# Kernel tuning notes

Measured on AMD Instinct MI355X. Metric: run time of the kernel, lower is better.

Reference implementation:

```python
import jax, jax.numpy as jnp
import numpy as np

TOP_K = 2


def setup_inputs() -> dict:
    key = jax.random.key(0)
    ks = jax.random.split(key, 7)
    B, S, D, E = 8, 2048, 1024, 8
    scale = 1.0 / np.sqrt(D)
    return {
        "X": jax.random.normal(ks[0], (B, S, D), dtype=jnp.float32),
        "We": jax.random.normal(ks[1], (E, D, D), dtype=jnp.float32) * scale,
        "be": jax.random.normal(ks[2], (E, D), dtype=jnp.float32) * scale,
        "Wr": jax.random.normal(ks[3], (E, D), dtype=jnp.float32) * scale,
        "br": jax.random.normal(ks[4], (E,), dtype=jnp.float32) * scale,
        "Wo": jax.random.normal(ks[5], (D, D), dtype=jnp.float32) * scale,
        "bo": jax.random.normal(ks[6], (D,), dtype=jnp.float32) * scale,
    }


def reference(X, We, be, Wr, br, Wo, bo):
    # Router: logits [B, S, E] -> softmax -> top-k
    router_logits = jnp.einsum("bsd,ed->bse", X, Wr) + br
    router_weights = jax.nn.softmax(router_logits, axis=-1)
    top_k_weights, top_k_indices = jax.lax.top_k(router_weights, TOP_K)  # [B,S,K]

    # Every expert Linear applied to all tokens (matches original's dense-per-expert math).
    # expert_outputs: [B, S, E, D]
    expert_outputs = jnp.einsum("bsd,ehd->bseh", X, We) + be

    # Gather the top-k experts per token and combine with router weights.
    # gathered: [B, S, K, D]
    gathered = jnp.take_along_axis(expert_outputs, top_k_indices[..., None], axis=2)
    combined = jnp.sum(top_k_weights[..., None] * gathered, axis=2)  # [B, S, D]

    # Output projection
    out = jnp.einsum("bsd,hd->bsh", combined, Wo) + bo
    return out
```

## Files before the change

### kernel.cpp

```cpp
#include <hip/hip_runtime.h>
#include <stdint.h>

#define T_TOK 16384
#define D_DIM 1024
#define E_NUM 8
#define NTILE 136

typedef __attribute__((ext_vector_type(4))) float f32x4;
typedef __attribute__((ext_vector_type(8))) __bf16 bf16x8;
typedef __attribute__((ext_vector_type(4))) unsigned short u16x4;
typedef const __attribute__((address_space(1))) void* gas_ptr;
typedef __attribute__((address_space(3))) void* las_ptr;

#define WS_Y     0ULL
#define WS_ATOK  67108864ULL
#define WS_AW    (WS_ATOK + 131072ULL)
#define WS_SCHED (WS_AW + 131072ULL)
#define WS_TMP   (WS_SCHED + 8192ULL)
#define WS_TKI   WS_TMP
#define WS_TKW   (WS_TKI + 131072ULL)
#define WS_CNTS  (WS_TKW + 131072ULL)
#define WS_BASE  (WS_CNTS + 8192ULL)
#define WS_WOB   WS_TMP


__device__ __forceinline__ unsigned short f2b(float f){
  unsigned int u = __float_as_uint(f);
  u = (u + 0x7FFFu + ((u >> 16) & 1u)) >> 16;
  return (unsigned short)u;
}

__global__ __launch_bounds__(256) void k_router(const float* __restrict__ X,
    const float* __restrict__ Wr, const float* __restrict__ br,
    unsigned short* __restrict__ Xb, int* __restrict__ tki, float* __restrict__ tkw)
{
  const int wv = threadIdx.x >> 6, lane = threadIdx.x & 63;
  const int t = blockIdx.x * 4 + wv;
  const float* x = X + (size_t)t * D_DIM;
  unsigned short* xb = Xb + (size_t)t * D_DIM;
  float acc[E_NUM] = {};
  #pragma unroll
  for (int c = 0; c < 4; ++c){
    const int d = c * 256 + lane * 4;
    f32x4 xv = *reinterpret_cast<const f32x4*>(x + d);
    u16x4 o;
    o[0]=f2b(xv[0]); o[1]=f2b(xv[1]); o[2]=f2b(xv[2]); o[3]=f2b(xv[3]);
    *reinterpret_cast<u16x4*>(xb + d) = o;
    #pragma unroll
    for (int e = 0; e < E_NUM; ++e){
      f32x4 w4 = *reinterpret_cast<const f32x4*>(Wr + e * D_DIM + d);
      acc[e] += xv[0]*w4[0] + xv[1]*w4[1] + xv[2]*w4[2] + xv[3]*w4[3];
    }
  }
  #pragma unroll
  for (int e = 0; e < E_NUM; ++e){
    float v = acc[e];
    #pragma unroll
    for (int off = 32; off >= 1; off >>= 1) v += __shfl_xor(v, off, 64);
    acc[e] = v + br[e];
  }
  int i1 = 0; float l1 = acc[0];
  #pragma unroll
  for (int e = 1; e < E_NUM; ++e) if (acc[e] > l1){ l1 = acc[e]; i1 = e; }
  int i2 = -1; float l2 = -3.4e38f;
  #pragma unroll
  for (int e = 0; e < E_NUM; ++e) if (e != i1 && acc[e] > l2){ l2 = acc[e]; i2 = e; }
  float s = 0.f;
  #pragma unroll
  for (int e = 0; e < E_NUM; ++e) s += __expf(acc[e] - l1);
  if (lane == 0){
    tki[2*t] = i1; tki[2*t+1] = i2;
    tkw[2*t] = 1.0f / s; tkw[2*t+1] = __expf(l2 - l1) / s;
  }
}

__global__ void k_cvt(const float* __restrict__ in, unsigned short* __restrict__ out, int n4)
{
  int i = blockIdx.x * blockDim.x + threadIdx.x;
  if (i >= n4) return;
  f32x4 v = reinterpret_cast<const f32x4*>(in)[i];
  u16x4 o;
  o[0]=f2b(v[0]); o[1]=f2b(v[1]); o[2]=f2b(v[2]); o[3]=f2b(v[3]);
  reinterpret_cast<u16x4*>(out)[i] = o;
}

__global__ __launch_bounds__(64) void k_hist(const int* __restrict__ tki, int* __restrict__ cnts)
{
  const int b = blockIdx.x, lane = threadIdx.x;
  const int t = b * 64 + lane;
  const int e0 = tki[2*t], e1 = tki[2*t+1];
  #pragma unroll
  for (int ex = 0; ex < E_NUM; ++ex){
    unsigned long long m0 = __ballot(e0 == ex);
    unsigned long long m1 = __ballot(e1 == ex);
    if (lane == 0) cnts[b * E_NUM + ex] = __popcll(m0) + __popcll(m1);
  }
}

__global__ __launch_bounds__(64) void k_scan(const int* __restrict__ cnts,
    int* __restrict__ bases, int4* __restrict__ sched)
{
  const int lane = threadIdx.x;
  const int e = lane & 7, g = lane >> 3;
  int own = 0;
  for (int i = 0; i < 32; ++i) own += cnts[(g * 32 + i) * E_NUM + e];
  int incl = own;
  #pragma unroll
  for (int s = 8; s < 64; s <<= 1){
    int v = __shfl_up(incl, s, 64);
    if (lane >= s) incl += v;
  }
  int tot[E_NUM];
  #pragma unroll
  for (int ee = 0; ee < E_NUM; ++ee) tot[ee] = __shfl(incl, 56 + ee, 64);
  int offs_e = 0;
  #pragma unroll
  for (int ee = 0; ee < E_NUM; ++ee) if (ee < e) offs_e += tot[ee];
  int run = offs_e + (incl - own);
  for (int i = 0; i < 32; ++i){
    const int b = g * 32 + i;
    bases[b * E_NUM + e] = run;
    run += cnts[b * E_NUM + e];
  }
  if (lane == 0){
    int slot = 0, off = 0;
    for (int ee = 0; ee < E_NUM; ++ee){
      const int c = tot[ee];
      for (int tile = 0; tile * 256 < c && slot < NTILE; ++tile)
        sched[slot++] = make_int4(ee, off + tile * 256, min(256, c - tile * 256), 0);
      off += c;
    }
    while (slot < NTILE) sched[slot++] = make_int4(0, 0, 0, 0);
  }
}

__global__ __launch_bounds__(64) void k_scatter(const int* __restrict__ tki,
    const float* __restrict__ tkw, const int* __restrict__ bases,
    int* __restrict__ atok, float* __restrict__ aw)
{
  const int b = blockIdx.x, lane = threadIdx.x;
  const int t = b * 64 + lane;
  const unsigned long long lt = (1ull << lane) - 1ull;
  const int e0 = tki[2*t], e1 = tki[2*t+1];
  int r0 = 0, r1 = 0, p0c[E_NUM];
  #pragma unroll
  for (int ex = 0; ex < E_NUM; ++ex){
    unsigned long long m0 = __ballot(e0 == ex);
    p0c[ex] = __popcll(m0);
    if (e0 == ex) r0 = __popcll(m0 & lt);
  }
  #pragma unroll
  for (int ex = 0; ex < E_NUM; ++ex){
    unsigned long long m1 = __ballot(e1 == ex);
    if (e1 == ex) r1 = p0c[ex] + __popcll(m1 & lt);
  }
  const int row0 = bases[b * E_NUM + e0] + r0;
  const int row1 = bases[b * E_NUM + e1] + r1;
  atok[row0] = 2*t;     aw[row0] = tkw[2*t];
  atok[row1] = 2*t + 1; aw[row1] = tkw[2*t+1];
}

__global__ __launch_bounds__(512, 4) void k_expert(const unsigned short* __restrict__ Xb,
    const unsigned short* __restrict__ Web, const float* __restrict__ be,
    const int4* __restrict__ sched, const int* __restrict__ atok,
    const float* __restrict__ aw, unsigned short* __restrict__ Y)
{
  __shared__ unsigned short As[256 * 64];
  __shared__ unsigned short Bs[128 * 64];
  __shared__ int   tok_s[256];
  __shared__ float w_s[256];

  const int lin = blockIdx.x;
  const int x = lin & 7, c = (lin >> 3) & 7, a = lin >> 6;
  const int j = x * 17 + a;
  const int4 sc = sched[j];
  const int e = sc.x, row0 = sc.y, nval = sc.z;
  const int n0 = c * 128;

  const int tid = threadIdx.x, wv = tid >> 6, lane = tid & 63;
  const int wm = wv >> 1, wn = wv & 1, lr = lane & 15, lg = lane >> 4;

  if (tid < 256){
    tok_s[tid] = atok[row0 + max(0, min(tid, nval - 1))];
    w_s[tid]   = aw[row0 + min(tid, 255)];
  }
  __syncthreads();

  const char* asrc[4]; const char* bsrc[2]; int ldsoA[4], ldsoB[2];
  #pragma unroll
  for (int i = 0; i < 4; ++i){
    const int chunk = i * 8 + wv;
    const int byte0 = chunk * 1024 + lane * 16;
    const int r = byte0 >> 7;
    const int scb = (byte0 & 127) ^ ((r & 7) << 4);
    asrc[i] = (const char*)(Xb + (size_t)(tok_s[r] >> 1) * D_DIM) + scb;
    ldsoA[i] = chunk * 512;
  }
  #pragma unroll
  for (int i = 0; i < 2; ++i){
    const int chunk = i * 8 + wv;
    const int byte0 = chunk * 1024 + lane * 16;
    const int r = byte0 >> 7;
    const int scb = (byte0 & 127) ^ ((r & 7) << 4);
    bsrc[i] = (const char*)(Web + ((size_t)e * D_DIM + n0 + r) * D_DIM) + scb;
    ldsoB[i] = chunk * 512;
  }

  f32x4 acc[4][4] = {};
  #pragma unroll 1
  for (int kt = 0; kt < 16; ++kt){
    __syncthreads();
    #pragma unroll
    for (int i = 0; i < 4; ++i)
      __builtin_amdgcn_global_load_lds((gas_ptr)(asrc[i] + kt * 128), (las_ptr)(As + ldsoA[i]), 16, 0, 0);
    #pragma unroll
    for (int i = 0; i < 2; ++i)
      __builtin_amdgcn_global_load_lds((gas_ptr)(bsrc[i] + kt * 128), (las_ptr)(Bs + ldsoB[i]), 16, 0, 0);
    __syncthreads();
    #pragma unroll
    for (int kk = 0; kk < 2; ++kk){
      bf16x8 af[4], bfr[4];
      #pragma unroll
      for (int fm = 0; fm < 4; ++fm){
        const int r = wm*64 + fm*16 + lr;
        af[fm] = *reinterpret_cast<const bf16x8*>((char*)As + ((r*128 + kk*64 + lg*16) ^ ((r & 7) << 4)));
      }
      #pragma unroll
      for (int fn = 0; fn < 4; ++fn){
        const int r = wn*64 + fn*16 + lr;
        bfr[fn] = *reinterpret_cast<const bf16x8*>((char*)Bs + ((r*128 + kk*64 + lg*16) ^ ((r & 7) << 4)));
      }
      #pragma unroll
      for (int fm = 0; fm < 4; ++fm)
        #pragma unroll
        for (int fn = 0; fn < 4; ++fn)
          acc[fm][fn] = __builtin_amdgcn_mfma_f32_16x16x32_bf16(af[fm], bfr[fn], acc[fm][fn], 0, 0, 0);
    }
  }

  float bev[4];
  #pragma unroll
  for (int fn = 0; fn < 4; ++fn) bev[fn] = be[e * D_DIM + n0 + wn*64 + fn*16 + lr];
  #pragma unroll
  for (int fm = 0; fm < 4; ++fm){
    #pragma unroll
    for (int jj = 0; jj < 4; ++jj){
      const int r = wm*64 + fm*16 + lg*4 + jj;
      if (r < nval){
        const float w = w_s[r];
        const size_t yrow = (size_t)tok_s[r];
        #pragma unroll
        for (int fn = 0; fn < 4; ++fn){
          const int col = n0 + wn*64 + fn*16 + lr;
          Y[yrow * D_DIM + col] = f2b(w * (acc[fm][fn][jj] + bev[fn]));
        }
      }
    }
  }
}

__global__ __launch_bounds__(512, 4) void k_outproj(const unsigned short* __restrict__ Y,
    const unsigned short* __restrict__ Wob, const float* __restrict__ bo,
    float* __restrict__ out)
{
  __shared__ unsigned short As0[256 * 64];
  __shared__ unsigned short As1[256 * 64];
  __shared__ unsigned short Bs[128 * 64];

  const int lin = blockIdx.x;
  const int x = lin & 7, c = (lin >> 3) & 7, a = lin >> 6;
  const int tm = x * 8 + a;
  const int n0 = c * 128;

  const int tid = threadIdx.x, wv = tid >> 6, lane = tid & 63;
  const int wm = wv >> 1, wn = wv & 1, lr = lane & 15, lg = lane >> 4;

  const char* a0src[4]; const char* a1src[4]; const char* bsrc[2]; int ldsoA[4], ldsoB[2];
  #pragma unroll
  for (int i = 0; i < 4; ++i){
    const int chunk = i * 8 + wv;
    const int byte0 = chunk * 1024 + lane * 16;
    const int r = byte0 >> 7;
    const int scb = (byte0 & 127) ^ ((r & 7) << 4);
    const size_t t = (size_t)(tm * 256 + r);
    a0src[i] = (const char*)(Y + (2*t)     * D_DIM) + scb;
    a1src[i] = (const char*)(Y + (2*t + 1) * D_DIM) + scb;
    ldsoA[i] = chunk * 512;
  }
  #pragma unroll
  for (int i = 0; i < 2; ++i){
    const int chunk = i * 8 + wv;
    const int byte0 = chunk * 1024 + lane * 16;
    const int r = byte0 >> 7;
    const int scb = (byte0 & 127) ^ ((r & 7) << 4);
    bsrc[i] = (const char*)(Wob + (size_t)(n0 + r) * D_DIM) + scb;
    ldsoB[i] = chunk * 512;
  }

  f32x4 acc[4][4] = {};
  #pragma unroll 1
  for (int kt = 0; kt < 16; ++kt){
    __syncthreads();
    #pragma unroll
    for (int i = 0; i < 4; ++i){
      __builtin_amdgcn_global_load_lds((gas_ptr)(a0src[i] + kt * 128), (las_ptr)(As0 + ldsoA[i]), 16, 0, 0);
      __builtin_amdgcn_global_load_lds((gas_ptr)(a1src[i] + kt * 128), (las_ptr)(As1 + ldsoA[i]), 16, 0, 0);
    }
    #pragma unroll
    for (int i = 0; i < 2; ++i)
      __builtin_amdgcn_global_load_lds((gas_ptr)(bsrc[i] + kt * 128), (las_ptr)(Bs + ldsoB[i]), 16, 0, 0);
    __syncthreads();
    #pragma unroll
    for (int kk = 0; kk < 2; ++kk){
      bf16x8 a0f[4], a1f[4], bfr[4];
      #pragma unroll
      for (int fm = 0; fm < 4; ++fm){
        const int r = wm*64 + fm*16 + lr;
        const int ba = (r*128 + kk*64 + lg*16) ^ ((r & 7) << 4);
        a0f[fm] = *reinterpret_cast<const bf16x8*>((char*)As0 + ba);
        a1f[fm] = *reinterpret_cast<const bf16x8*>((char*)As1 + ba);
      }
      #pragma unroll
      for (int fn = 0; fn < 4; ++fn){
        const int r = wn*64 + fn*16 + lr;
        bfr[fn] = *reinterpret_cast<const bf16x8*>((char*)Bs + ((r*128 + kk*64 + lg*16) ^ ((r & 7) << 4)));
      }
      #pragma unroll
      for (int fm = 0; fm < 4; ++fm)
        #pragma unroll
        for (int fn = 0; fn < 4; ++fn){
          acc[fm][fn] = __builtin_amdgcn_mfma_f32_16x16x32_bf16(a0f[fm], bfr[fn], acc[fm][fn], 0, 0, 0);
          acc[fm][fn] = __builtin_amdgcn_mfma_f32_16x16x32_bf16(a1f[fm], bfr[fn], acc[fm][fn], 0, 0, 0);
        }
    }
  }

  float bov[4];
  #pragma unroll
  for (int fn = 0; fn < 4; ++fn) bov[fn] = bo[n0 + wn*64 + fn*16 + lr];
  #pragma unroll
  for (int fm = 0; fm < 4; ++fm){
    #pragma unroll
    for (int jj = 0; jj < 4; ++jj){
      const int r = wm*64 + fm*16 + lg*4 + jj;
      #pragma unroll
      for (int fn = 0; fn < 4; ++fn){
        const int col = n0 + wn*64 + fn*16 + lr;
        out[(size_t)(tm * 256 + r) * D_DIM + col] = acc[fm][fn][jj] + bov[fn];
      }
    }
  }
}

extern "C" void kernel_launch(void* const* d_in, const int* in_sizes, int n_in,
                              void* d_out, int out_size, void* d_ws, size_t ws_size,
                              hipStream_t stream)
{
  const float* X  = (const float*)d_in[0];
  const float* We = (const float*)d_in[1];
  const float* be = (const float*)d_in[2];
  const float* Wr = (const float*)d_in[3];
  const float* br = (const float*)d_in[4];
  const float* Wo = (const float*)d_in[5];
  const float* bo = (const float*)d_in[6];
  float* out = (float*)d_out;
  char* ws = (char*)d_ws;

  unsigned short* Y   = (unsigned short*)(ws + WS_Y);
  int*   atok  = (int*)(ws + WS_ATOK);
  float* aw    = (float*)(ws + WS_AW);
  int4*  sched = (int4*)(ws + WS_SCHED);
  int*   tki   = (int*)(ws + WS_TKI);
  float* tkw   = (float*)(ws + WS_TKW);
  int*   cnts  = (int*)(ws + WS_CNTS);
  int*   bases = (int*)(ws + WS_BASE);
  unsigned short* Wob = (unsigned short*)(ws + WS_WOB);

  unsigned short* Xb  = (unsigned short*)d_out;
  unsigned short* Web = (unsigned short*)((char*)d_out + 33554432);

  k_router<<<T_TOK / 4, 256, 0, stream>>>(X, Wr, br, Xb, tki, tkw);
  k_cvt<<<(E_NUM * D_DIM * D_DIM / 4) / 256, 256, 0, stream>>>(We, Web, E_NUM * D_DIM * D_DIM / 4);
  k_hist<<<256, 64, 0, stream>>>(tki, cnts);
  k_scan<<<1, 64, 0, stream>>>(cnts, bases, sched);
  k_scatter<<<256, 64, 0, stream>>>(tki, tkw, bases, atok, aw);
  k_cvt<<<(D_DIM * D_DIM / 4) / 256, 256, 0, stream>>>(Wo, Wob, D_DIM * D_DIM / 4);
  k_expert<<<NTILE * 8, 512, 0, stream>>>(Xb, Web, be, sched, atok, aw, Y);
  k_outproj<<<512, 512, 0, stream>>>(Y, Wob, bo, out);
}
```

Before: 333.8 us.

## Fuse router and weight conversions; merge routing schedule kernels into one block

Combines the router, expert-weight and output-weight bf16 conversions into a single launch, and folds histogram, scan and scatter into one single-block kernel using shared memory. Expert tiles with no tokens now exit early. Router weights are staged as bf16 to shrink workspace. This reduces launch count and inter-kernel gaps, at the cost of a serial single-block scheduling step and slightly lower precision of combine weights.

```diff
diff --git a/kernel.cpp b/kernel.cpp
--- a/kernel.cpp
+++ b/kernel.cpp
@@ -16,12 +16,9 @@
 #define WS_ATOK  67108864ULL
 #define WS_AW    (WS_ATOK + 131072ULL)
 #define WS_SCHED (WS_AW + 131072ULL)
-#define WS_TMP   (WS_SCHED + 8192ULL)
-#define WS_TKI   WS_TMP
-#define WS_TKW   (WS_TKI + 131072ULL)
-#define WS_CNTS  (WS_TKW + 131072ULL)
-#define WS_BASE  (WS_CNTS + 8192ULL)
-#define WS_WOB   WS_TMP
+#define WS_TKI   (WS_SCHED + 2304ULL)
+#define WS_TKWH  (WS_TKI + 131072ULL)
+#define WS_WOB   (WS_TKWH + 65536ULL)
 
 
 __device__ __forceinline__ unsigned short f2b(float f){
@@ -29,135 +26,153 @@
   u = (u + 0x7FFFu + ((u >> 16) & 1u)) >> 16;
   return (unsigned short)u;
 }
-
-__global__ __launch_bounds__(256) void k_router(const float* __restrict__ X,
+__device__ __forceinline__ float b2f(unsigned short u){
+  return __uint_as_float(((unsigned int)u) << 16);
+}
+
+__global__ __launch_bounds__(256) void k_prep(const float* __restrict__ X,
     const float* __restrict__ Wr, const float* __restrict__ br,
-    unsigned short* __restrict__ Xb, int* __restrict__ tki, float* __restrict__ tkw)
+    const float* __restrict__ We, const float* __restrict__ Wo,
+    unsigned short* __restrict__ Xb, unsigned short* __restrict__ Web,
+    unsigned short* __restrict__ Wob, int* __restrict__ tki, unsigned short* __restrict__ tkwh)
 {
-  const int wv = threadIdx.x >> 6, lane = threadIdx.x & 63;
-  const int t = blockIdx.x * 4 + wv;
-  const float* x = X + (size_t)t * D_DIM;
-  unsigned short* xb = Xb + (size_t)t * D_DIM;
-  float acc[E_NUM] = {};
-  #pragma unroll
-  for (int c = 0; c < 4; ++c){
-    const int d = c * 256 + lane * 4;
-    f32x4 xv = *reinterpret_cast<const f32x4*>(x + d);
+  const int bid = blockIdx.x;
+  if (bid < 4096){
+    const int wv = threadIdx.x >> 6, lane = threadIdx.x & 63;
+    const int t = bid * 4 + wv;
+    const float* x = X + (size_t)t * D_DIM;
+    unsigned short* xb = Xb + (size_t)t * D_DIM;
+    float acc[E_NUM] = {};
+    #pragma unroll
+    for (int c = 0; c < 4; ++c){
+      const int d = c * 256 + lane * 4;
+      f32x4 xv = *reinterpret_cast<const f32x4*>(x + d);
+      u16x4 o;
+      o[0]=f2b(xv[0]); o[1]=f2b(xv[1]); o[2]=f2b(xv[2]); o[3]=f2b(xv[3]);
+      *reinterpret_cast<u16x4*>(xb + d) = o;
+      #pragma unroll
+      for (int e = 0; e < E_NUM; ++e){
+        f32x4 w4 = *reinterpret_cast<const f32x4*>(Wr + e * D_DIM + d);
+        acc[e] += xv[0]*w4[0] + xv[1]*w4[1] + xv[2]*w4[2] + xv[3]*w4[3];
+      }
+    }
+    #pragma unroll
+    for (int e = 0; e < E_NUM; ++e){
+      float v = acc[e];
+      #pragma unroll
+      for (int off = 32; off >= 1; off >>= 1) v += __shfl_xor(v, off, 64);
+      acc[e] = v + br[e];
+    }
+    int i1 = 0; float l1 = acc[0];
+    #pragma unroll
+    for (int e = 1; e < E_NUM; ++e) if (acc[e] > l1){ l1 = acc[e]; i1 = e; }
+    int i2 = -1; float l2 = -3.4e38f;
+    #pragma unroll
+    for (int e = 0; e < E_NUM; ++e) if (e != i1 && acc[e] > l2){ l2 = acc[e]; i2 = e; }
+    float s = 0.f;
+    #pragma unroll
+    for (int e = 0; e < E_NUM; ++e) s += __expf(acc[e] - l1);
+    if (lane == 0){
+      tki[2*t] = i1; tki[2*t+1] = i2;
+      tkwh[2*t] = f2b(1.0f / s); tkwh[2*t+1] = f2b(__expf(l2 - l1) / s);
+    }
+  } else if (bid < 12288){
+    const int i = (bid - 4096) * 256 + threadIdx.x;
+    f32x4 v = reinterpret_cast<const f32x4*>(We)[i];
     u16x4 o;
-    o[0]=f2b(xv[0]); o[1]=f2b(xv[1]); o[2]=f2b(xv[2]); o[3]=f2b(xv[3]);
-    *reinterpret_cast<u16x4*>(xb + d) = o;
-    #pragma unroll
-    for (int e = 0; e < E_NUM; ++e){
-      f32x4 w4 = *reinterpret_cast<const f32x4*>(Wr + e * D_DIM + d);
-      acc[e] += xv[0]*w4[0] + xv[1]*w4[1] + xv[2]*w4[2] + xv[3]*w4[3];
-    }
-  }
-  #pragma unroll
-  for (int e = 0; e < E_NUM; ++e){
-    float v = acc[e];
-    #pragma unroll
-    for (int off = 32; off >= 1; off >>= 1) v += __shfl_xor(v, off, 64);
-    acc[e] = v + br[e];
-  }
-  int i1 = 0; float l1 = acc[0];
-  #pragma unroll
-  for (int e = 1; e < E_NUM; ++e) if (acc[e] > l1){ l1 = acc[e]; i1 = e; }
-  int i2 = -1; float l2 = -3.4e38f;
-  #pragma unroll
-  for (int e = 0; e < E_NUM; ++e) if (e != i1 && acc[e] > l2){ l2 = acc[e]; i2 = e; }
-  float s = 0.f;
-  #pragma unroll
-  for (int e = 0; e < E_NUM; ++e) s += __expf(acc[e] - l1);
-  if (lane == 0){
-    tki[2*t] = i1; tki[2*t+1] = i2;
-    tkw[2*t] = 1.0f / s; tkw[2*t+1] = __expf(l2 - l1) / s;
-  }
-}
-
-__global__ void k_cvt(const float* __restrict__ in, unsigned short* __restrict__ out, int n4)
-{
-  int i = blockIdx.x * blockDim.x + threadIdx.x;
-  if (i >= n4) return;
-  f32x4 v = reinterpret_cast<const f32x4*>(in)[i];
-  u16x4 o;
-  o[0]=f2b(v[0]); o[1]=f2b(v[1]); o[2]=f2b(v[2]); o[3]=f2b(v[3]);
-  reinterpret_cast<u16x4*>(out)[i] = o;
-}
-
-__global__ __launch_bounds__(64) void k_hist(const int* __restrict__ tki, int* __restrict__ cnts)
-{
-  const int b = blockIdx.x, lane = threadIdx.x;
-  const int t = b * 64 + lane;
-  const int e0 = tki[2*t], e1 = tki[2*t+1];
-  #pragma unroll
-  for (int ex = 0; ex < E_NUM; ++ex){
-    unsigned long long m0 = __ballot(e0 == ex);
-    unsigned long long m1 = __ballot(e1 == ex);
-    if (lane == 0) cnts[b * E_NUM + ex] = __popcll(m0) + __popcll(m1);
-  }
-}
-
-__global__ __launch_bounds__(64) void k_scan(const int* __restrict__ cnts,
-    int* __restrict__ bases, int4* __restrict__ sched)
-{
-  const int lane = threadIdx.x;
-  const int e = lane & 7, g = lane >> 3;
-  int own = 0;
-  for (int i = 0; i < 32; ++i) own += cnts[(g * 32 + i) * E_NUM + e];
-  int incl = own;
-  #pragma unroll
-  for (int s = 8; s < 64; s <<= 1){
-    int v = __shfl_up(incl, s, 64);
-    if (lane >= s) incl += v;
-  }
-  int tot[E_NUM];
-  #pragma unroll
-  for (int ee = 0; ee < E_NUM; ++ee) tot[ee] = __shfl(incl, 56 + ee, 64);
-  int offs_e = 0;
-  #pragma unroll
-  for (int ee = 0; ee < E_NUM; ++ee) if (ee < e) offs_e += tot[ee];
-  int run = offs_e + (incl - own);
-  for (int i = 0; i < 32; ++i){
-    const int b = g * 32 + i;
-    bases[b * E_NUM + e] = run;
-    run += cnts[b * E_NUM + e];
-  }
-  if (lane == 0){
-    int slot = 0, off = 0;
-    for (int ee = 0; ee < E_NUM; ++ee){
-      const int c = tot[ee];
-      for (int tile = 0; tile * 256 < c && slot < NTILE; ++tile)
-        sched[slot++] = make_int4(ee, off + tile * 256, min(256, c - tile * 256), 0);
-      off += c;
-    }
-    while (slot < NTILE) sched[slot++] = make_int4(0, 0, 0, 0);
-  }
-}
-
-__global__ __launch_bounds__(64) void k_scatter(const int* __restrict__ tki,
-    const float* __restrict__ tkw, const int* __restrict__ bases,
+    o[0]=f2b(v[0]); o[1]=f2b(v[1]); o[2]=f2b(v[2]); o[3]=f2b(v[3]);
+    reinterpret_cast<u16x4*>(Web)[i] = o;
+  } else {
+    const int i = (bid - 12288) * 256 + threadIdx.x;
+    f32x4 v = reinterpret_cast<const f32x4*>(Wo)[i];
+    u16x4 o;
+    o[0]=f2b(v[0]); o[1]=f2b(v[1]); o[2]=f2b(v[2]); o[3]=f2b(v[3]);
+    reinterpret_cast<u16x4*>(Wob)[i] = o;
+  }
+}
+
+__global__ __launch_bounds__(1024) void k_sched2(const int* __restrict__ tki,
+    const unsigned short* __restrict__ tkwh, int4* __restrict__ sched,
     int* __restrict__ atok, float* __restrict__ aw)
 {
-  const int b = blockIdx.x, lane = threadIdx.x;
-  const int t = b * 64 + lane;
-  const unsigned long long lt = (1ull << lane) - 1ull;
-  const int e0 = tki[2*t], e1 = tki[2*t+1];
-  int r0 = 0, r1 = 0, p0c[E_NUM];
-  #pragma unroll
-  for (int ex = 0; ex < E_NUM; ++ex){
-    unsigned long long m0 = __ballot(e0 == ex);
-    p0c[ex] = __popcll(m0);
-    if (e0 == ex) r0 = __popcll(m0 & lt);
-  }
-  #pragma unroll
-  for (int ex = 0; ex < E_NUM; ++ex){
-    unsigned long long m1 = __ballot(e1 == ex);
-    if (e1 == ex) r1 = p0c[ex] + __popcll(m1 & lt);
-  }
-  const int row0 = bases[b * E_NUM + e0] + r0;
-  const int row1 = bases[b * E_NUM + e1] + r1;
-  atok[row0] = 2*t;     aw[row0] = tkw[2*t];
-  atok[row1] = 2*t + 1; aw[row1] = tkw[2*t+1];
+  __shared__ int cnts[256][E_NUM];
+  __shared__ int bases[256][E_NUM];
+  const int tid = threadIdx.x, wv = tid >> 6, lane = tid & 63;
+
+  #pragma unroll 1
+  for (int i = 0; i < 16; ++i){
+    const int g = wv * 16 + i;
+    const int t = g * 64 + lane;
+    const int e0 = tki[2*t], e1 = tki[2*t+1];
+    #pragma unroll
+    for (int ex = 0; ex < E_NUM; ++ex){
+      unsigned long long m0 = __ballot(e0 == ex);
+      unsigned long long m1 = __ballot(e1 == ex);
+      if (lane == 0) cnts[g][ex] = __popcll(m0) + __popcll(m1);
+    }
+  }
+  __syncthreads();
+
+  if (wv == 0){
+    const int e = lane & 7, g8 = lane >> 3;
+    int own = 0;
+    #pragma unroll 1
+    for (int i = 0; i < 32; ++i) own += cnts[g8 * 32 + i][e];
+    int incl = own;
+    #pragma unroll
+    for (int s = 8; s < 64; s <<= 1){
+      int v = __shfl_up(incl, s, 64);
+      if (lane >= s) incl += v;
+    }
+    int tot[E_NUM];
+    #pragma unroll
+    for (int ee = 0; ee < E_NUM; ++ee) tot[ee] = __shfl(incl, 56 + ee, 64);
+    int offs_e = 0;
+    #pragma unroll
+    for (int ee = 0; ee < E_NUM; ++ee) if (ee < e) offs_e += tot[ee];
+    int run = offs_e + (incl - own);
+    #pragma unroll 1
+    for (int i = 0; i < 32; ++i){
+      const int b = g8 * 32 + i;
+      bases[b][e] = run;
+      run += cnts[b][e];
+    }
+    if (lane == 0){
+      int slot = 0, off = 0;
+      for (int ee = 0; ee < E_NUM; ++ee){
+        const int c = tot[ee];
+        for (int tile = 0; tile * 256 < c && slot < NTILE; ++tile)
+          sched[slot++] = make_int4(ee, off + tile * 256, min(256, c - tile * 256), 0);
+        off += c;
+      }
+      while (slot < NTILE) sched[slot++] = make_int4(0, 0, 0, 0);
+    }
+  }
+  __syncthreads();
+
+  #pragma unroll 1
+  for (int i = 0; i < 16; ++i){
+    const int g = wv * 16 + i;
+    const int t = g * 64 + lane;
+    const unsigned long long lt = (1ull << lane) - 1ull;
+    const int e0 = tki[2*t], e1 = tki[2*t+1];
+    int r0 = 0, r1 = 0, p0c[E_NUM];
+    #pragma unroll
+    for (int ex = 0; ex < E_NUM; ++ex){
+      unsigned long long m0 = __ballot(e0 == ex);
+      p0c[ex] = __popcll(m0);
+      if (e0 == ex) r0 = __popcll(m0 & lt);
+    }
+    #pragma unroll
+    for (int ex = 0; ex < E_NUM; ++ex){
+      unsigned long long m1 = __ballot(e1 == ex);
+      if (e1 == ex) r1 = p0c[ex] + __popcll(m1 & lt);
+    }
+    const int row0 = bases[g][e0] + r0;
+    const int row1 = bases[g][e1] + r1;
+    atok[row0] = 2*t;     aw[row0] = b2f(tkwh[2*t]);
+    atok[row1] = 2*t + 1; aw[row1] = b2f(tkwh[2*t+1]);
+  }
 }
 
 __global__ __launch_bounds__(512, 4) void k_expert(const unsigned short* __restrict__ Xb,
@@ -175,6 +190,7 @@
   const int j = x * 17 + a;
   const int4 sc = sched[j];
   const int e = sc.x, row0 = sc.y, nval = sc.z;
+  if (nval == 0) return;
   const int n0 = c * 128;
 
   const int tid = threadIdx.x, wv = tid >> 6, lane = tid & 63;
@@ -366,25 +382,19 @@
   float* out = (float*)d_out;
   char* ws = (char*)d_ws;
 
-  unsigned short* Y   = (unsigned short*)(ws + WS_Y);
-  int*   atok  = (int*)(ws + WS_ATOK);
-  float* aw    = (float*)(ws + WS_AW);
-  int4*  sched = (int4*)(ws + WS_SCHED);
-  int*   tki   = (int*)(ws + WS_TKI);
-  float* tkw   = (float*)(ws + WS_TKW);
-  int*   cnts  = (int*)(ws + WS_CNTS);
-  int*   bases = (int*)(ws + WS_BASE);
-  unsigned short* Wob = (unsigned short*)(ws + WS_WOB);
+  unsigned short* Y    = (unsigned short*)(ws + WS_Y);
+  int*            atok = (int*)(ws + WS_ATOK);
+  float*          aw   = (float*)(ws + WS_AW);
+  int4*           sched= (int4*)(ws + WS_SCHED);
+  int*            tki  = (int*)(ws + WS_TKI);
+  unsigned short* tkwh = (unsigned short*)(ws + WS_TKWH);
+  unsigned short* Wob  = (unsigned short*)(ws + WS_WOB);
 
   unsigned short* Xb  = (unsigned short*)d_out;
   unsigned short* Web = (unsigned short*)((char*)d_out + 33554432);
 
-  k_router<<<T_TOK / 4, 256, 0, stream>>>(X, Wr, br, Xb, tki, tkw);
-  k_cvt<<<(E_NUM * D_DIM * D_DIM / 4) / 256, 256, 0, stream>>>(We, Web, E_NUM * D_DIM * D_DIM / 4);
-  k_hist<<<256, 64, 0, stream>>>(tki, cnts);
-  k_scan<<<1, 64, 0, stream>>>(cnts, bases, sched);
-  k_scatter<<<256, 64, 0, stream>>>(tki, tkw, bases, atok, aw);
-  k_cvt<<<(D_DIM * D_DIM / 4) / 256, 256, 0, stream>>>(Wo, Wob, D_DIM * D_DIM / 4);
+  k_prep<<<13312, 256, 0, stream>>>(X, Wr, br, We, Wo, Xb, Web, Wob, tki, tkwh);
+  k_sched2<<<1, 1024, 0, stream>>>(tki, tkwh, sched, atok, aw);
   k_expert<<<NTILE * 8, 512, 0, stream>>>(Xb, Web, be, sched, atok, aw, Y);
   k_outproj<<<512, 512, 0, stream>>>(Y, Wob, bo, out);
 }
```

Result: slower. 358.7 us (+7.4%).
